# Kernel optimization log

Hardware: AMD Instinct MI355X
Metric: run time of the kernel (lower is better)

The kernel has to match this reference:

```python
import jax, jax.numpy as jnp
import numpy as np

SERIES_LEN = 4096
D_EMB = 1024
D_V = 1024
HURST = 0.7
H = HURST - 0.5          # exponent used by the module
DT = 1.0 / SERIES_LEN
EPS = 1e-8


def _attn_matrix():
    # Lower-triangular fractional power-law matrix A2[i, j]:
    #   j <  i : ((i - j) * dt + 1e-8) ** (hurst - 0.5)
    #   j == i : 1e-8 ** (hurst - 0.5)
    #   j >  i : 0
    i = jnp.arange(SERIES_LEN, dtype=jnp.int32)[:, None]
    j = jnp.arange(SERIES_LEN, dtype=jnp.int32)[None, :]
    diff = jnp.clip(i - j, 1, None).astype(jnp.float32)  # safe base for fractional power
    lower = jnp.where(i > j, (diff * DT + EPS) ** H, 0.0)
    diag = jnp.eye(SERIES_LEN, dtype=jnp.float32) * (EPS ** H)
    return lower + diag  # (L, L) float32


def setup_inputs() -> dict:
    key = jax.random.key(0)
    k1, k2 = jax.random.split(key)
    embed_series = jax.random.normal(k1, (D_EMB, SERIES_LEN), dtype=jnp.float32)
    # nn.Linear(d_emb, d_v, bias=False) weight has shape (d_v, d_emb)
    Wv_weight = jax.random.normal(k2, (D_V, D_EMB), dtype=jnp.float32) * (1.0 / np.sqrt(D_EMB))
    return {"embed_series": embed_series, "Wv_weight": Wv_weight}


def reference(embed_series, Wv_weight):
    # V (original, d_v x L) = Wv(embed_series.T).T ; output[i, c] = sum_j A2[i, j] * V[c, j]
    # => out = A2 @ (embed_series.T @ Wv_weight.T), shape (L, d_v)
    A2 = _attn_matrix()                                   # (L, L) lower triangular
    Y = jnp.einsum('el,ve->lv', embed_series, Wv_weight)  # (L, d_v)
    return A2 @ Y                                         # (L, d_v)
```

## Files before the change

kernel.cpp:

```cpp
#include <hip/hip_runtime.h>
#include <hip/hip_bf16.h>
#include <cstdint>
#include <cstddef>


#define L_SER 4096
#define DEMB  1024
#define DV    1024

#define R_STRIDE 4224
#define R_O0     4096

typedef __bf16 bf16_t;
typedef __attribute__((ext_vector_type(8))) __bf16 bf16x8;
typedef __attribute__((ext_vector_type(4))) float f32x4;

__device__ __forceinline__ void glds16(const bf16_t* g, bf16_t* l) {
    __builtin_amdgcn_global_load_lds(
        (const __attribute__((address_space(1))) unsigned int*)(const void*)g,
        (__attribute__((address_space(3))) unsigned int*)(void*)l,
        16, 0, 0);
}

__global__ void prep_kernel(const float* __restrict__ E, const float* __restrict__ W,
                            bf16_t* __restrict__ Eb, bf16_t* __restrict__ Wb,
                            bf16_t* __restrict__ R) {
    const int b = blockIdx.x;
    if (b < 132) {
        int idx = b * 256 + threadIdx.x;
        int s = idx / R_STRIDE;
        int x = idx - s * R_STRIDE;
        int d = R_O0 + s - x;
        float v = 0.0f;
        if (d >= 0 && d < L_SER)
            v = powf((d == 0) ? 1e-8f : ((float)d * (1.0f / (float)L_SER) + 1e-8f), 0.2f);
        R[idx] = (bf16_t)v;
    } else if (b < 132 + 2048) {
        int idx = (b - 132) * 256 + threadIdx.x;
        const f32x4* s = (const f32x4*)E;
        f32x4 v0 = s[idx * 2], v1 = s[idx * 2 + 1];
        bf16x8 o;
        o[0] = (bf16_t)v0[0]; o[1] = (bf16_t)v0[1]; o[2] = (bf16_t)v0[2]; o[3] = (bf16_t)v0[3];
        o[4] = (bf16_t)v1[0]; o[5] = (bf16_t)v1[1]; o[6] = (bf16_t)v1[2]; o[7] = (bf16_t)v1[3];
        ((bf16x8*)Eb)[idx] = o;
    } else {
        int idx = (b - 2180) * 256 + threadIdx.x;
        const f32x4* s = (const f32x4*)W;
        f32x4 v0 = s[idx * 2], v1 = s[idx * 2 + 1];
        bf16x8 o;
        o[0] = (bf16_t)v0[0]; o[1] = (bf16_t)v0[1]; o[2] = (bf16_t)v0[2]; o[3] = (bf16_t)v0[3];
        o[4] = (bf16_t)v1[0]; o[5] = (bf16_t)v1[1]; o[6] = (bf16_t)v1[2]; o[7] = (bf16_t)v1[3];
        ((bf16x8*)Wb)[idx] = o;
    }
}

#define GA_LANES()                                                           \
    const int tid  = threadIdx.x;                                            \
    const int wave = tid >> 6;                                               \
    const int lane = tid & 63;                                               \
    const int quad = lane >> 4;                                              \
    const int ln   = lane & 15;                                              \
    const int wm   = wave >> 1;                                              \
    const int wn   = wave & 1;                                               \
    const int lrow = lane >> 3;                                              \
    const int lch  = (lane & 7) ^ lrow;                                      \
    const int rsw   = ln & 7;                                                \
    const int coff0 = ((quad ^ rsw)) * 8;                                    \
    const int coff1 = (((4 + quad) ^ rsw)) * 8;

#define GA_STAGE_B(SBOFS)                                                    \
    _Pragma("unroll")                                                        \
    for (int c = 0; c < 4; ++c) {                                            \
        glds16(pB[c], &sB[(SBOFS) + (c * 32 + wave * 8) * 64]);              \
        pB[c] += 64;                                                         \
    }

#define GA_COMPUTE(SBOFS)                                                    \
    _Pragma("unroll")                                                        \
    for (int kk = 0; kk < 2; ++kk) {                                         \
        const int co = kk ? coff1 : coff0;                                   \
        bf16x8 afr[4], bfr[4];                                               \
        _Pragma("unroll")                                                    \
        for (int tm = 0; tm < 4; ++tm)                                       \
            afr[tm] = *(const bf16x8*)(pRA + (kk * 32 + quad * 8 - 16 * tm)); \
        _Pragma("unroll")                                                    \
        for (int tn = 0; tn < 4; ++tn)                                       \
            bfr[tn] = *(const bf16x8*)&sB[(SBOFS) + (wn * 64 + tn * 16 + ln) * 64 + co]; \
        _Pragma("unroll")                                                    \
        for (int tm = 0; tm < 4; ++tm)                                       \
            _Pragma("unroll")                                                \
            for (int tn = 0; tn < 4; ++tn)                                   \
                acc[tm][tn] = __builtin_amdgcn_mfma_f32_16x16x32_bf16(afr[tm], bfr[tn], acc[tm][tn], 0, 0, 0); \
    }                                                                        \
    pRA += 64;

__global__ __launch_bounds__(256, 2) void gemm_a_kernel(const bf16_t* __restrict__ R,
                                                        const bf16_t* __restrict__ Eb,
                                                        bf16_t* __restrict__ T0,
                                                        bf16_t* __restrict__ T1) {
    __shared__ __align__(16) bf16_t sB[2 * 128 * 64];

    const int bid = blockIdx.x;
    int I, nb, h;
    if (bid < 256) { I = bid >> 3;                nb = bid & 7;         h = 0; }
    else           { I = 31 - ((bid - 256) >> 3); nb = (bid - 256) & 7; h = 1; }
    const int i0 = I * 128;
    const int n0 = nb * 128;
    const int nsteps = I + 1;
    const int j0b = h ? 64 * (I + 1) : 0;
    bf16_t* __restrict__ Tout = h ? T1 : T0;

    GA_LANES()

    f32x4 acc[4][4];
#pragma unroll
    for (int a = 0; a < 4; ++a)
#pragma unroll
        for (int b = 0; b < 4; ++b) acc[a][b] = (f32x4){0, 0, 0, 0};

    const bf16_t* pRA = R + (size_t)(ln & 7) * R_STRIDE +
                        (R_O0 - i0 + j0b - 64 * wm - 8 * (ln >> 3) + 48);
    pRA -= 48;

    const bf16_t* pB[4];
#pragma unroll
    for (int c = 0; c < 4; ++c)
        pB[c] = Eb + (size_t)(n0 + c * 32 + wave * 8 + lrow) * L_SER + j0b + lch * 8;

    GA_STAGE_B(0)
    for (int s = 0;; s += 2) {
        __syncthreads();
        if (s + 1 < nsteps) { GA_STAGE_B(128 * 64) }
        GA_COMPUTE(0)
        if (s + 1 >= nsteps) break;
        __syncthreads();
        if (s + 2 < nsteps) { GA_STAGE_B(0) }
        GA_COMPUTE(128 * 64)
        if (s + 2 >= nsteps) break;
    }

#pragma unroll
    for (int tm = 0; tm < 4; ++tm) {
        int row_base = i0 + wm * 64 + tm * 16 + quad * 4;
#pragma unroll
        for (int tn = 0; tn < 4; ++tn) {
            int col = n0 + wn * 64 + tn * 16 + ln;
#pragma unroll
            for (int r = 0; r < 4; ++r)
                Tout[(size_t)(row_base + r) * DEMB + col] = (bf16_t)acc[tm][tn][r];
        }
    }
}

#define GB_STAGE_A(SBOFS)                                                    \
    _Pragma("unroll")                                                        \
    for (int c = 0; c < 4; ++c) {                                            \
        glds16(pA[c], &sA[(SBOFS) + (c * 32 + wave * 8) * 64]);              \
        pA[c] += 64;                                                         \
    }

#define GB_COMPUTE(SBOFS)                                                    \
    _Pragma("unroll")                                                        \
    for (int kk = 0; kk < 2; ++kk) {                                         \
        const int co = kk ? coff1 : coff0;                                   \
        bf16x8 afr[4], bfr[4];                                               \
        _Pragma("unroll")                                                    \
        for (int c = 0; c < 4; ++c)                                          \
            afr[c] = *(const bf16x8*)&sA[(SBOFS) + (((c >> 1) * 64) + wm * 32 + (c & 1) * 16 + ln) * 64 + co]; \
        _Pragma("unroll")                                                    \
        for (int tn = 0; tn < 4; ++tn)                                       \
            bfr[tn] = *(const bf16x8*)(pWg[tn] + kk * 32 + quad * 8);        \
        _Pragma("unroll")                                                    \
        for (int t = 0; t < 2; ++t)                                          \
            _Pragma("unroll")                                                \
            for (int tn = 0; tn < 4; ++tn)                                   \
                acc[t][tn] = __builtin_amdgcn_mfma_f32_16x16x32_bf16(afr[t], bfr[tn], acc[t][tn], 0, 0, 0); \
        _Pragma("unroll")                                                    \
        for (int t = 0; t < 2; ++t)                                          \
            _Pragma("unroll")                                                \
            for (int tn = 0; tn < 4; ++tn)                                   \
                acc[t][tn] = __builtin_amdgcn_mfma_f32_16x16x32_bf16(afr[2 + t], bfr[tn], acc[t][tn], 0, 0, 0); \
    }                                                                        \
    _Pragma("unroll")                                                        \
    for (int tn = 0; tn < 4; ++tn) pWg[tn] += 64;

__global__ __launch_bounds__(256, 2) void gemm_b_kernel(const bf16_t* __restrict__ T0,
                                                        const bf16_t* __restrict__ T1,
                                                        const bf16_t* __restrict__ Wb,
                                                        float* __restrict__ out) {
    __shared__ __align__(16) bf16_t sA[2 * 128 * 64];

    const int bid = blockIdx.x;
    const int ib = bid >> 3;
    const int nb = bid & 7;
    const int i0 = ib * 64;
    const int n0 = nb * 128;

    GA_LANES()

    f32x4 acc[2][4];
#pragma unroll
    for (int a = 0; a < 2; ++a)
#pragma unroll
        for (int b = 0; b < 4; ++b) acc[a][b] = (f32x4){0, 0, 0, 0};

    const int nsteps = DEMB / 64;

    const bf16_t* pA[4];
#pragma unroll
    for (int c = 0; c < 4; ++c) {
        const bf16_t* base = (c < 2) ? T0 : T1;
        int rr = (c & 1) * 32 + wave * 8 + lrow;
        pA[c] = base + (size_t)(i0 + rr) * DEMB + lch * 8;
    }
    const bf16_t* pWg[4];
#pragma unroll
    for (int tn = 0; tn < 4; ++tn)
        pWg[tn] = Wb + (size_t)(n0 + wn * 64 + tn * 16 + ln) * DEMB;

    GB_STAGE_A(0)
    for (int s = 0;; s += 2) {
        __syncthreads();
        if (s + 1 < nsteps) { GB_STAGE_A(128 * 64) }
        GB_COMPUTE(0)
        if (s + 1 >= nsteps) break;
        __syncthreads();
        if (s + 2 < nsteps) { GB_STAGE_A(0) }
        GB_COMPUTE(128 * 64)
        if (s + 2 >= nsteps) break;
    }

#pragma unroll
    for (int t = 0; t < 2; ++t) {
        int row_base = i0 + wm * 32 + t * 16 + quad * 4;
#pragma unroll
        for (int tn = 0; tn < 4; ++tn) {
            int col = n0 + wn * 64 + tn * 16 + ln;
#pragma unroll
            for (int r = 0; r < 4; ++r)
                out[(size_t)(row_base + r) * DV + col] = acc[t][tn][r];
        }
    }
}

extern "C" void kernel_launch(void* const* d_in, const int* in_sizes, int n_in,
                              void* d_out, int out_size, void* d_ws, size_t ws_size,
                              hipStream_t stream) {
    const float* E = (const float*)d_in[0];
    const float* W = (const float*)d_in[1];
    float* out = (float*)d_out;

    char* ws = (char*)d_ws;
    bf16_t* Eb = (bf16_t*)(ws);
    bf16_t* T0 = (bf16_t*)(ws + (size_t)8  * 1024 * 1024);
    bf16_t* T1 = (bf16_t*)(ws + (size_t)16 * 1024 * 1024);
    bf16_t* Wb = (bf16_t*)(ws + (size_t)24 * 1024 * 1024);
    bf16_t* R  = (bf16_t*)(ws + (size_t)26 * 1024 * 1024);

    prep_kernel<<<2692, 256, 0, stream>>>(E, W, Eb, Wb, R);
    gemm_a_kernel<<<512, 256, 0, stream>>>(R, Eb, T0, T1);
    gemm_b_kernel<<<512, 256, 0, stream>>>(T0, T1, Wb, out);
}
```

Before: 146.8 us.

## Stage Toeplitz window and W operand through LDS in both GEMMs

In gemm_a, the A operand (a window of the Toeplitz row table R) is now loaded into a small double-buffered LDS window with async global-to-LDS copies, instead of being read straight from global memory per fragment. In gemm_b, the W operand is likewise staged into a second double-buffered LDS tile alongside the T tiles, replacing direct global loads. The R table grows slightly (two more prep blocks) so the window loads stay in bounds. The aim is to cut scattered, uncoalesced global reads in the inner loop. The cost is extra LDS use (gemm_b shared memory doubles), which may limit occupancy at two blocks per CU.

```diff
diff --git a/kernel.cpp b/kernel.cpp
--- a/kernel.cpp
+++ b/kernel.cpp
@@ -26,7 +26,7 @@
                             bf16_t* __restrict__ Eb, bf16_t* __restrict__ Wb,
                             bf16_t* __restrict__ R) {
     const int b = blockIdx.x;
-    if (b < 132) {
+    if (b < 134) {
         int idx = b * 256 + threadIdx.x;
         int s = idx / R_STRIDE;
         int x = idx - s * R_STRIDE;
@@ -35,8 +35,8 @@
         if (d >= 0 && d < L_SER)
             v = powf((d == 0) ? 1e-8f : ((float)d * (1.0f / (float)L_SER) + 1e-8f), 0.2f);
         R[idx] = (bf16_t)v;
-    } else if (b < 132 + 2048) {
-        int idx = (b - 132) * 256 + threadIdx.x;
+    } else if (b < 134 + 2048) {
+        int idx = (b - 134) * 256 + threadIdx.x;
         const f32x4* s = (const f32x4*)E;
         f32x4 v0 = s[idx * 2], v1 = s[idx * 2 + 1];
         bf16x8 o;
@@ -44,7 +44,7 @@
         o[4] = (bf16_t)v1[0]; o[5] = (bf16_t)v1[1]; o[6] = (bf16_t)v1[2]; o[7] = (bf16_t)v1[3];
         ((bf16x8*)Eb)[idx] = o;
     } else {
-        int idx = (b - 2180) * 256 + threadIdx.x;
+        int idx = (b - 2182) * 256 + threadIdx.x;
         const f32x4* s = (const f32x4*)W;
         f32x4 v0 = s[idx * 2], v1 = s[idx * 2 + 1];
         bf16x8 o;
@@ -68,21 +68,23 @@
     const int coff0 = ((quad ^ rsw)) * 8;                                    \
     const int coff1 = (((4 + quad) ^ rsw)) * 8;
 
-#define GA_STAGE_B(SBOFS)                                                    \
+#define GA_STAGE(SBOFS, WOFS)                                                \
     _Pragma("unroll")                                                        \
     for (int c = 0; c < 4; ++c) {                                            \
         glds16(pB[c], &sB[(SBOFS) + (c * 32 + wave * 8) * 64]);              \
         pB[c] += 64;                                                         \
-    }
-
-#define GA_COMPUTE(SBOFS)                                                    \
+    }                                                                        \
+    glds16(pRwin, &sW[(WOFS) + wave * 512]);                                 \
+    pRwin += 64;
+
+#define GA_COMPUTE(SBOFS, WOFS)                                              \
     _Pragma("unroll")                                                        \
     for (int kk = 0; kk < 2; ++kk) {                                         \
         const int co = kk ? coff1 : coff0;                                   \
         bf16x8 afr[4], bfr[4];                                               \
         _Pragma("unroll")                                                    \
         for (int tm = 0; tm < 4; ++tm)                                       \
-            afr[tm] = *(const bf16x8*)(pRA + (kk * 32 + quad * 8 - 16 * tm)); \
+            afr[tm] = *(const bf16x8*)&sW[(WOFS) + awbase + (kk * 32 + quad * 8 - 16 * tm)]; \
         _Pragma("unroll")                                                    \
         for (int tn = 0; tn < 4; ++tn)                                       \
             bfr[tn] = *(const bf16x8*)&sB[(SBOFS) + (wn * 64 + tn * 16 + ln) * 64 + co]; \
@@ -91,14 +93,14 @@
             _Pragma("unroll")                                                \
             for (int tn = 0; tn < 4; ++tn)                                   \
                 acc[tm][tn] = __builtin_amdgcn_mfma_f32_16x16x32_bf16(afr[tm], bfr[tn], acc[tm][tn], 0, 0, 0); \
-    }                                                                        \
-    pRA += 64;
+    }
 
 __global__ __launch_bounds__(256, 2) void gemm_a_kernel(const bf16_t* __restrict__ R,
                                                         const bf16_t* __restrict__ Eb,
                                                         bf16_t* __restrict__ T0,
                                                         bf16_t* __restrict__ T1) {
     __shared__ __align__(16) bf16_t sB[2 * 128 * 64];
+    __shared__ __align__(16) bf16_t sW[2 * 2048];
 
     const int bid = blockIdx.x;
     int I, nb, h;
@@ -112,30 +114,32 @@
 
     GA_LANES()
 
+    const int awbase = (ln & 7) * 200 + 120 - 64 * wm - 8 * (ln >> 3);
+
     f32x4 acc[4][4];
 #pragma unroll
     for (int a = 0; a < 4; ++a)
 #pragma unroll
         for (int b = 0; b < 4; ++b) acc[a][b] = (f32x4){0, 0, 0, 0};
 
-    const bf16_t* pRA = R + (size_t)(ln & 7) * R_STRIDE +
-                        (R_O0 - i0 + j0b - 64 * wm - 8 * (ln >> 3) + 48);
-    pRA -= 48;
+    const int wrow = tid / 25;
+    const int wchk = tid - wrow * 25;
+    const bf16_t* pRwin = R + (size_t)wrow * R_STRIDE + (R_O0 - i0 + j0b - 120 + wchk * 8);
 
     const bf16_t* pB[4];
 #pragma unroll
     for (int c = 0; c < 4; ++c)
         pB[c] = Eb + (size_t)(n0 + c * 32 + wave * 8 + lrow) * L_SER + j0b + lch * 8;
 
-    GA_STAGE_B(0)
+    GA_STAGE(0, 0)
     for (int s = 0;; s += 2) {
         __syncthreads();
-        if (s + 1 < nsteps) { GA_STAGE_B(128 * 64) }
-        GA_COMPUTE(0)
+        if (s + 1 < nsteps) { GA_STAGE(128 * 64, 2048) }
+        GA_COMPUTE(0, 0)
         if (s + 1 >= nsteps) break;
         __syncthreads();
-        if (s + 2 < nsteps) { GA_STAGE_B(0) }
-        GA_COMPUTE(128 * 64)
+        if (s + 2 < nsteps) { GA_STAGE(0, 0) }
+        GA_COMPUTE(128 * 64, 2048)
         if (s + 2 >= nsteps) break;
     }
 
@@ -152,11 +156,12 @@
     }
 }
 
-#define GB_STAGE_A(SBOFS)                                                    \
+#define GB_STAGE(SBOFS)                                                      \
     _Pragma("unroll")                                                        \
     for (int c = 0; c < 4; ++c) {                                            \
         glds16(pA[c], &sA[(SBOFS) + (c * 32 + wave * 8) * 64]);              \
-        pA[c] += 64;                                                         \
+        glds16(pW[c], &sBB[(SBOFS) + (c * 32 + wave * 8) * 64]);             \
+        pA[c] += 64; pW[c] += 64;                                            \
     }
 
 #define GB_COMPUTE(SBOFS)                                                    \
@@ -169,7 +174,7 @@
             afr[c] = *(const bf16x8*)&sA[(SBOFS) + (((c >> 1) * 64) + wm * 32 + (c & 1) * 16 + ln) * 64 + co]; \
         _Pragma("unroll")                                                    \
         for (int tn = 0; tn < 4; ++tn)                                       \
-            bfr[tn] = *(const bf16x8*)(pWg[tn] + kk * 32 + quad * 8);        \
+            bfr[tn] = *(const bf16x8*)&sBB[(SBOFS) + (wn * 64 + tn * 16 + ln) * 64 + co]; \
         _Pragma("unroll")                                                    \
         for (int t = 0; t < 2; ++t)                                          \
             _Pragma("unroll")                                                \
@@ -180,15 +185,14 @@
             _Pragma("unroll")                                                \
             for (int tn = 0; tn < 4; ++tn)                                   \
                 acc[t][tn] = __builtin_amdgcn_mfma_f32_16x16x32_bf16(afr[2 + t], bfr[tn], acc[t][tn], 0, 0, 0); \
-    }                                                                        \
-    _Pragma("unroll")                                                        \
-    for (int tn = 0; tn < 4; ++tn) pWg[tn] += 64;
+    }
 
 __global__ __launch_bounds__(256, 2) void gemm_b_kernel(const bf16_t* __restrict__ T0,
                                                         const bf16_t* __restrict__ T1,
                                                         const bf16_t* __restrict__ Wb,
                                                         float* __restrict__ out) {
     __shared__ __align__(16) bf16_t sA[2 * 128 * 64];
+    __shared__ __align__(16) bf16_t sBB[2 * 128 * 64];
 
     const int bid = blockIdx.x;
     const int ib = bid >> 3;
@@ -207,25 +211,23 @@
     const int nsteps = DEMB / 64;
 
     const bf16_t* pA[4];
+    const bf16_t* pW[4];
 #pragma unroll
     for (int c = 0; c < 4; ++c) {
         const bf16_t* base = (c < 2) ? T0 : T1;
         int rr = (c & 1) * 32 + wave * 8 + lrow;
         pA[c] = base + (size_t)(i0 + rr) * DEMB + lch * 8;
-    }
-    const bf16_t* pWg[4];
-#pragma unroll
-    for (int tn = 0; tn < 4; ++tn)
-        pWg[tn] = Wb + (size_t)(n0 + wn * 64 + tn * 16 + ln) * DEMB;
-
-    GB_STAGE_A(0)
+        pW[c] = Wb + (size_t)(n0 + c * 32 + wave * 8 + lrow) * DEMB + lch * 8;
+    }
+
+    GB_STAGE(0)
     for (int s = 0;; s += 2) {
         __syncthreads();
-        if (s + 1 < nsteps) { GB_STAGE_A(128 * 64) }
+        if (s + 1 < nsteps) { GB_STAGE(128 * 64) }
         GB_COMPUTE(0)
         if (s + 1 >= nsteps) break;
         __syncthreads();
-        if (s + 2 < nsteps) { GB_STAGE_A(0) }
+        if (s + 2 < nsteps) { GB_STAGE(0) }
         GB_COMPUTE(128 * 64)
         if (s + 2 >= nsteps) break;
     }
@@ -257,7 +259,7 @@
     bf16_t* Wb = (bf16_t*)(ws + (size_t)24 * 1024 * 1024);
     bf16_t* R  = (bf16_t*)(ws + (size_t)26 * 1024 * 1024);
 
-    prep_kernel<<<2692, 256, 0, stream>>>(E, W, Eb, Wb, R);
+    prep_kernel<<<2694, 256, 0, stream>>>(E, W, Eb, Wb, R);
     gemm_a_kernel<<<512, 256, 0, stream>>>(R, Eb, T0, T1);
     gemm_b_kernel<<<512, 256, 0, stream>>>(T0, T1, Wb, out);
 }
```

Measured after the change: 123.3 us. 16.0% less time.
